# Kernel optimization log

Hardware: AMD Instinct MI355X
Metric: run time of the kernel (lower is better)

## Reference

```python
import jax, jax.numpy as jnp
import numpy as np

V, H, B = 64, 128, 16384  # num_visible, num_hidden = alpha*V, batch of spin configs
ISCALE = 0.001


def setup_inputs() -> dict:
    key = jax.random.key(0)
    k1, k2, k3, k4 = jax.random.split(key, 4)
    x = jax.random.normal(k1, (B, V), dtype=jnp.float32)
    weight_1 = jax.random.normal(k2, (V, H), dtype=jnp.float32) * ISCALE
    weight_2 = jax.random.normal(k3, (H, V, V), dtype=jnp.float32) * (ISCALE / 10.0)
    hidden_bias = jax.random.normal(k4, (H,), dtype=jnp.float32) * ISCALE
    return {"x": x, "weight_1": weight_1, "weight_2": weight_2, "hidden_bias": hidden_bias}


def reference(x, weight_1, weight_2, hidden_bias):
    b, v = x.shape
    h = weight_2.shape[0]
    # order-1 term: (B,V) @ (V,H) -> (B,H)
    w1 = x @ weight_1
    # order-2 term: outer product of spins per sample, contracted with weight_2.
    # vis_ij: (B,V,V) flattened to (B,V*V); weight_2 flattened to (H,V*V) -> GEMM.
    vis_ij = jnp.einsum('mi,mj->mij', x, x).reshape(b, v * v)
    w2 = (vis_ij @ weight_2.reshape(h, v * v).T) * 0.5
    act = jnp.cos(hidden_bias + w1 + w2)  # (B,H)
    psi = jnp.prod(act, axis=-1)          # (B,)
    return psi
```

## Files before the change

### kernel.cpp

```cpp
#include <hip/hip_runtime.h>
#include <hip/hip_bf16.h>
#include <cstdint>

#define NV 64
#define NH 128
#define NB 16384
#define NCHUNK 37
#define FRAG_ELEMS (NCHUNK * 8192)

typedef __bf16 bf16x8_t __attribute__((ext_vector_type(8)));
typedef float f32x4_t __attribute__((ext_vector_type(4)));
typedef float f32x2_t __attribute__((ext_vector_type(2)));
typedef uint32_t u32x4_t __attribute__((ext_vector_type(4)));
typedef uint32_t u32x2_t __attribute__((ext_vector_type(2)));

__device__ __forceinline__ uint32_t bf16_rne(float f) {
  uint32_t u = __float_as_uint(f);
  return (u + 0x7fffu + ((u >> 16) & 1u)) >> 16;
}

__global__ void cvt_kernel(const float* __restrict__ w1f,
                           const float* __restrict__ w2f,
                           uint16_t* __restrict__ frag) {
  int tg = blockIdx.x * 256 + threadIdx.x;
  int l = tg & 63, fh = (tg >> 6) & 7, c2 = tg >> 9;
  int chunk = c2 >> 1, jh = c2 & 1;
  int h = fh * 16 + (l & 15);
  int kb = jh * 32 + (l >> 4) * 8;
  uint32_t o16[8];
#pragma unroll
  for (int t = 0; t < 8; ++t) {
    int slot = kb + t;
    float v;
    if (chunk < 8) {
      int i = chunk * 8 + (slot >> 3), j = chunk * 8 + (slot & 7);
      v = 0.5f * w2f[h * 4096 + i * 64 + j];
    } else if (chunk < 36) {
      int o = chunk - 8, I = 0;
      while (o >= 7 - I) { o -= 7 - I; ++I; }
      int J = I + 1 + o;
      int i = I * 8 + (slot >> 3), j = J * 8 + (slot & 7);
      v = 0.5f * (w2f[h * 4096 + i * 64 + j] + w2f[h * 4096 + j * 64 + i]);
    } else {
      v = w1f[slot * 128 + h];
    }
    o16[t] = bf16_rne(v);
  }
  uint4 o;
  o.x = (o16[1] << 16) | o16[0];
  o.y = (o16[3] << 16) | o16[2];
  o.z = (o16[5] << 16) | o16[4];
  o.w = (o16[7] << 16) | o16[6];
  *(uint4*)(frag + ((size_t)(c2 * 8 + fh) << 9) + l * 8) = o;
}

__launch_bounds__(512, 2)
__global__ void rbm_kernel(const float* __restrict__ xg,
                           const float* __restrict__ biasg,
                           const __hip_bfloat16* __restrict__ frag,
                           float* __restrict__ outg) {
  __shared__ __align__(16) float xtile[64 * 76];
  __shared__ float part[4][64];

  const int tid  = threadIdx.x;
  const int wv   = tid >> 6;
  const int wm   = wv & 1;
  const int hq   = wv >> 1;
  const int lane = tid & 63;
  const int c15  = lane & 15;
  const int q    = lane >> 4;
  const int mblk = blockIdx.x * 64;

  constexpr int CI[36] = {0,1,2,3,4,5,6,7, 0,0,0,0,0,0,0, 1,1,1,1,1,1,
                          2,2,2,2,2, 3,3,3,3, 4,4,4, 5,5, 6};
  constexpr int CJ[36] = {0,1,2,3,4,5,6,7, 1,2,3,4,5,6,7, 2,3,4,5,6,7,
                          3,4,5,6,7, 4,5,6,7, 5,6,7, 6,7, 7};

  {
    int row = tid >> 3, grp = tid & 7;
    const float* p = xg + (size_t)(mblk + row) * NV + grp * 8;
    float4 a = *(const float4*)(p);
    float4 b = *(const float4*)(p + 4);
    *(float4*)(&xtile[row * 76 + grp * 8]) = a;
    *(float4*)(&xtile[row * 76 + grp * 8 + 4]) = b;
    xtile[row * 76 + 64 + grp] = 1.0f;
  }
  __syncthreads();

  const float* sx[2];
  f32x2_t xb[2][32];
#pragma unroll
  for (int im = 0; im < 2; ++im) {
    sx[im] = &xtile[(wm * 32 + im * 16 + c15) * 76];
#pragma unroll
    for (int g = 0; g < 8; ++g) {
      float4 a = *(const float4*)(sx[im] + g * 8);
      float4 b = *(const float4*)(sx[im] + g * 8 + 4);
      xb[im][g * 4 + 0] = f32x2_t{a.x, a.y};
      xb[im][g * 4 + 1] = f32x2_t{a.z, a.w};
      xb[im][g * 4 + 2] = f32x2_t{b.x, b.y};
      xb[im][g * 4 + 3] = f32x2_t{b.z, b.w};
    }
  }

  const __hip_bfloat16* pw = frag + (size_t)hq * 1024 + lane * 8;

  f32x4_t acc[2][2];
#pragma unroll
  for (int im = 0; im < 2; ++im)
#pragma unroll
    for (int ih = 0; ih < 2; ++ih)
      acc[im][ih] = (f32x4_t)0.0f;

  bf16x8_t bn[2][2];
#pragma unroll
  for (int jh = 0; jh < 2; ++jh)
#pragma unroll
    for (int ih = 0; ih < 2; ++ih)
      bn[jh][ih] = *(const bf16x8_t*)(pw + jh * 4096 + ih * 512);

#pragma unroll
  for (int c = 0; c < 36; ++c) {
    bf16x8_t bc[2][2];
#pragma unroll
    for (int jh = 0; jh < 2; ++jh)
#pragma unroll
      for (int ih = 0; ih < 2; ++ih)
        bc[jh][ih] = bn[jh][ih];
    {
      const __hip_bfloat16* pn = pw + (size_t)(c + 1) * 8192;
#pragma unroll
      for (int jh = 0; jh < 2; ++jh)
#pragma unroll
        for (int ih = 0; ih < 2; ++ih)
          bn[jh][ih] = *(const bf16x8_t*)(pn + jh * 4096 + ih * 512);
    }
    const int I = CI[c], J = CJ[c];
#pragma unroll
    for (int jh = 0; jh < 2; ++jh) {
      bf16x8_t afrag[2];
#pragma unroll
      for (int im = 0; im < 2; ++im) {
        float s = sx[im][I * 8 + jh * 4 + q];
        const f32x2_t s2 = f32x2_t{s, s};
        u32x4_t adv;
#pragma unroll
        for (int tt = 0; tt < 4; ++tt) {
          f32x2_t pr = s2 * xb[im][J * 4 + tt];
          u32x2_t u = __builtin_bit_cast(u32x2_t, pr);
          adv[tt] = __builtin_amdgcn_perm(u[1], u[0], 0x07060302);
        }
        afrag[im] = __builtin_bit_cast(bf16x8_t, adv);
      }
#pragma unroll
      for (int ih = 0; ih < 2; ++ih)
#pragma unroll
        for (int im = 0; im < 2; ++im)
          acc[im][ih] = __builtin_amdgcn_mfma_f32_16x16x32_bf16(
              afrag[im], bc[jh][ih], acc[im][ih], 0, 0, 0);
    }
  }

#pragma unroll
  for (int jh = 0; jh < 2; ++jh) {
    bf16x8_t afrag[2];
#pragma unroll
    for (int im = 0; im < 2; ++im) {
      float4 a = *(const float4*)(sx[im] + jh * 32 + q * 8);
      float4 b = *(const float4*)(sx[im] + jh * 32 + q * 8 + 4);
      const float pr[4][2] = {{a.x, a.y}, {a.z, a.w}, {b.x, b.y}, {b.z, b.w}};
      u32x4_t adv;
#pragma unroll
      for (int tt = 0; tt < 4; ++tt)
        adv[tt] = __builtin_amdgcn_perm(__float_as_uint(pr[tt][1]),
                                        __float_as_uint(pr[tt][0]), 0x07060302);
      afrag[im] = __builtin_bit_cast(bf16x8_t, adv);
    }
#pragma unroll
    for (int ih = 0; ih < 2; ++ih)
#pragma unroll
      for (int im = 0; im < 2; ++im)
        acc[im][ih] = __builtin_amdgcn_mfma_f32_16x16x32_bf16(
            afrag[im], bn[jh][ih], acc[im][ih], 0, 0, 0);
  }

  float bs[2];
#pragma unroll
  for (int ih = 0; ih < 2; ++ih)
    bs[ih] = biasg[hq * 32 + ih * 16 + c15];

  const float INV2PI = 0.15915494309189535f;
  float prod[2][4];
#pragma unroll
  for (int im = 0; im < 2; ++im)
#pragma unroll
    for (int r = 0; r < 4; ++r) {
      float c0 = __builtin_amdgcn_cosf((acc[im][0][r] + bs[0]) * INV2PI);
      float c1 = __builtin_amdgcn_cosf((acc[im][1][r] + bs[1]) * INV2PI);
      prod[im][r] = c0 * c1;
    }

#pragma unroll
  for (int ofs = 1; ofs < 16; ofs <<= 1)
#pragma unroll
    for (int im = 0; im < 2; ++im)
#pragma unroll
      for (int r = 0; r < 4; ++r)
        prod[im][r] *= __shfl_xor(prod[im][r], ofs, 16);

  if (c15 == 0) {
#pragma unroll
    for (int im = 0; im < 2; ++im)
#pragma unroll
      for (int r = 0; r < 4; ++r)
        part[hq][wm * 32 + im * 16 + q * 4 + r] = prod[im][r];
  }
  __syncthreads();
  if (tid < 64) {
    float f = part[0][tid] * part[1][tid] * part[2][tid] * part[3][tid];
    outg[mblk + tid] = f;
  }
}

extern "C" void kernel_launch(void* const* d_in, const int* in_sizes, int n_in,
                              void* d_out, int out_size, void* d_ws, size_t ws_size,
                              hipStream_t stream) {
  const float* x   = (const float*)d_in[0];
  const float* w1f = (const float*)d_in[1];
  const float* w2f = (const float*)d_in[2];
  const float* hb  = (const float*)d_in[3];
  float* out = (float*)d_out;
  uint16_t* frag = (uint16_t*)d_ws;
  (void)in_sizes; (void)n_in; (void)out_size; (void)ws_size;

  cvt_kernel<<<148, 256, 0, stream>>>(w1f, w2f, frag);
  rbm_kernel<<<NB / 64, 512, 0, stream>>>(
      x, hb, (const __hip_bfloat16*)frag, out);
}
```

Baseline: 85.98 us.

## Split-K across two blocks with 32x32 MFMA and separate cos-product reduction

The main kernel now splits the 37-chunk K dimension across two blocks per M tile using blockIdx.y. Each block uses 32x32x16 MFMA with a single accumulator, and partial sums go to a workspace buffer P. A third kernel adds the two partials and bias, applies cos, and does the row product with wave shuffles. The weight-conversion kernel stages each hidden unit's W2 slice in shared memory and writes a new fragment layout. This doubles grid parallelism and raises occupancy, at the cost of about 16 MB of extra partial-sum traffic and an extra kernel launch.

```diff
diff --git a/kernel.cpp b/kernel.cpp
--- a/kernel.cpp
+++ b/kernel.cpp
@@ -6,10 +6,9 @@
 #define NH 128
 #define NB 16384
 #define NCHUNK 37
-#define FRAG_ELEMS (NCHUNK * 8192)
 
 typedef __bf16 bf16x8_t __attribute__((ext_vector_type(8)));
-typedef float f32x4_t __attribute__((ext_vector_type(4)));
+typedef float f32x16_t __attribute__((ext_vector_type(16)));
 typedef float f32x2_t __attribute__((ext_vector_type(2)));
 typedef uint32_t u32x4_t __attribute__((ext_vector_type(4)));
 typedef uint32_t u32x2_t __attribute__((ext_vector_type(2)));
@@ -21,204 +20,173 @@
 
 __global__ void cvt_kernel(const float* __restrict__ w1f,
                            const float* __restrict__ w2f,
-                           uint16_t* __restrict__ frag) {
-  int tg = blockIdx.x * 256 + threadIdx.x;
-  int l = tg & 63, fh = (tg >> 6) & 7, c2 = tg >> 9;
-  int chunk = c2 >> 1, jh = c2 & 1;
-  int h = fh * 16 + (l & 15);
-  int kb = jh * 32 + (l >> 4) * 8;
-  uint32_t o16[8];
-#pragma unroll
-  for (int t = 0; t < 8; ++t) {
-    int slot = kb + t;
-    float v;
-    if (chunk < 8) {
-      int i = chunk * 8 + (slot >> 3), j = chunk * 8 + (slot & 7);
-      v = 0.5f * w2f[h * 4096 + i * 64 + j];
-    } else if (chunk < 36) {
-      int o = chunk - 8, I = 0;
+                           uint8_t* __restrict__ frag) {
+  __shared__ float W[4096];
+  __shared__ float w1c[64];
+  const int tid = threadIdx.x;
+  const int h = blockIdx.x;
+  {
+    const float* src = w2f + (size_t)h * 4096;
+#pragma unroll
+    for (int u = 0; u < 4; ++u)
+      *(float4*)(&W[u * 1024 + tid * 4]) =
+          *(const float4*)(src + u * 1024 + tid * 4);
+  }
+  if (tid < 64) w1c[tid] = w1f[tid * 128 + h];
+  __syncthreads();
+  const int fh2 = h >> 5, hl = h & 31;
+  for (int idx = tid; idx < 296; idx += 256) {
+    int c = idx >> 3, kk = (idx >> 1) & 3, lh = idx & 1;
+    int a = kk * 2 + lh;
+    float v[8];
+    if (c < 8) {
+      int ib = (c * 8 + a) * 64 + c * 8;
+#pragma unroll
+      for (int t = 0; t < 8; ++t) v[t] = 0.5f * W[ib + t];
+    } else if (c < 36) {
+      int o = c - 8, I = 0;
       while (o >= 7 - I) { o -= 7 - I; ++I; }
       int J = I + 1 + o;
-      int i = I * 8 + (slot >> 3), j = J * 8 + (slot & 7);
-      v = 0.5f * (w2f[h * 4096 + i * 64 + j] + w2f[h * 4096 + j * 64 + i]);
+      int i = I * 8 + a;
+#pragma unroll
+      for (int t = 0; t < 8; ++t) {
+        int j = J * 8 + t;
+        v[t] = 0.5f * (W[i * 64 + j] + W[j * 64 + i]);
+      }
     } else {
-      v = w1f[slot * 128 + h];
-    }
-    o16[t] = bf16_rne(v);
-  }
-  uint4 o;
-  o.x = (o16[1] << 16) | o16[0];
-  o.y = (o16[3] << 16) | o16[2];
-  o.z = (o16[5] << 16) | o16[4];
-  o.w = (o16[7] << 16) | o16[6];
-  *(uint4*)(frag + ((size_t)(c2 * 8 + fh) << 9) + l * 8) = o;
-}
-
-__launch_bounds__(512, 2)
-__global__ void rbm_kernel(const float* __restrict__ xg,
-                           const float* __restrict__ biasg,
-                           const __hip_bfloat16* __restrict__ frag,
-                           float* __restrict__ outg) {
-  __shared__ __align__(16) float xtile[64 * 76];
-  __shared__ float part[4][64];
-
-  const int tid  = threadIdx.x;
-  const int wv   = tid >> 6;
-  const int wm   = wv & 1;
-  const int hq   = wv >> 1;
-  const int lane = tid & 63;
-  const int c15  = lane & 15;
-  const int q    = lane >> 4;
-  const int mblk = blockIdx.x * 64;
-
+      int sb = kk * 16 + lh * 8;
+#pragma unroll
+      for (int t = 0; t < 8; ++t) v[t] = w1c[sb + t];
+    }
+    uint4 o4;
+    o4.x = (bf16_rne(v[1]) << 16) | bf16_rne(v[0]);
+    o4.y = (bf16_rne(v[3]) << 16) | bf16_rne(v[2]);
+    o4.z = (bf16_rne(v[5]) << 16) | bf16_rne(v[4]);
+    o4.w = (bf16_rne(v[7]) << 16) | bf16_rne(v[6]);
+    *(uint4*)(frag + ((size_t)((c * 4 + kk) * 4 + fh2) << 10) +
+              ((lh * 32 + hl) << 4)) = o4;
+  }
+}
+
+__device__ __forceinline__ uint32_t pack2(f32x2_t pr) {
+  u32x2_t u = __builtin_bit_cast(u32x2_t, pr);
+  return __builtin_amdgcn_perm(u[1], u[0], 0x07060302);
+}
+
+template <int C0, int C1>
+__device__ __forceinline__ void kloop(const uint8_t* pw, const f32x2_t* xb,
+                                      int lh, f32x16_t& acc, bf16x8_t* bn) {
   constexpr int CI[36] = {0,1,2,3,4,5,6,7, 0,0,0,0,0,0,0, 1,1,1,1,1,1,
                           2,2,2,2,2, 3,3,3,3, 4,4,4, 5,5, 6};
   constexpr int CJ[36] = {0,1,2,3,4,5,6,7, 1,2,3,4,5,6,7, 2,3,4,5,6,7,
                           3,4,5,6,7, 4,5,6,7, 5,6,7, 6,7, 7};
-
+#pragma unroll
+  for (int c = C0; c < C1; ++c) {
+    bf16x8_t bc[4];
+#pragma unroll
+    for (int kk = 0; kk < 4; ++kk) bc[kk] = bn[kk];
+    const uint8_t* pn = pw + (size_t)(c + 1) * 16384;
+#pragma unroll
+    for (int kk = 0; kk < 4; ++kk)
+      bn[kk] = *(const bf16x8_t*)(pn + kk * 4096);
+    const int I = CI[c], J = CJ[c];
+#pragma unroll
+    for (int kk = 0; kk < 4; ++kk) {
+      f32x2_t sp = xb[I * 4 + kk];
+      float s = lh ? sp.y : sp.x;
+      f32x2_t s2 = {s, s};
+      u32x4_t adv;
+#pragma unroll
+      for (int tt = 0; tt < 4; ++tt)
+        adv[tt] = pack2(s2 * xb[J * 4 + tt]);
+      acc = __builtin_amdgcn_mfma_f32_32x32x16_bf16(
+          __builtin_bit_cast(bf16x8_t, adv), bc[kk], acc, 0, 0, 0);
+    }
+  }
+}
+
+__launch_bounds__(512, 4)
+__global__ void rbm_main(const float* __restrict__ xg,
+                         const uint8_t* __restrict__ frag,
+                         float* __restrict__ P) {
+  const int tid = threadIdx.x;
+  const int wv = tid >> 6;
+  const int wm = wv & 1;
+  const int hq = wv >> 1;
+  const int lane = tid & 63;
+  const int l31 = lane & 31;
+  const int lh = lane >> 5;
+  const int mblk = blockIdx.x * 64;
+  const int ks = blockIdx.y;
+
+  f32x2_t xb[32];
   {
-    int row = tid >> 3, grp = tid & 7;
-    const float* p = xg + (size_t)(mblk + row) * NV + grp * 8;
-    float4 a = *(const float4*)(p);
-    float4 b = *(const float4*)(p + 4);
-    *(float4*)(&xtile[row * 76 + grp * 8]) = a;
-    *(float4*)(&xtile[row * 76 + grp * 8 + 4]) = b;
-    xtile[row * 76 + 64 + grp] = 1.0f;
-  }
-  __syncthreads();
-
-  const float* sx[2];
-  f32x2_t xb[2][32];
-#pragma unroll
-  for (int im = 0; im < 2; ++im) {
-    sx[im] = &xtile[(wm * 32 + im * 16 + c15) * 76];
-#pragma unroll
-    for (int g = 0; g < 8; ++g) {
-      float4 a = *(const float4*)(sx[im] + g * 8);
-      float4 b = *(const float4*)(sx[im] + g * 8 + 4);
-      xb[im][g * 4 + 0] = f32x2_t{a.x, a.y};
-      xb[im][g * 4 + 1] = f32x2_t{a.z, a.w};
-      xb[im][g * 4 + 2] = f32x2_t{b.x, b.y};
-      xb[im][g * 4 + 3] = f32x2_t{b.z, b.w};
-    }
-  }
-
-  const __hip_bfloat16* pw = frag + (size_t)hq * 1024 + lane * 8;
-
-  f32x4_t acc[2][2];
-#pragma unroll
-  for (int im = 0; im < 2; ++im)
-#pragma unroll
-    for (int ih = 0; ih < 2; ++ih)
-      acc[im][ih] = (f32x4_t)0.0f;
-
-  bf16x8_t bn[2][2];
-#pragma unroll
-  for (int jh = 0; jh < 2; ++jh)
-#pragma unroll
-    for (int ih = 0; ih < 2; ++ih)
-      bn[jh][ih] = *(const bf16x8_t*)(pw + jh * 4096 + ih * 512);
-
-#pragma unroll
-  for (int c = 0; c < 36; ++c) {
-    bf16x8_t bc[2][2];
-#pragma unroll
-    for (int jh = 0; jh < 2; ++jh)
-#pragma unroll
-      for (int ih = 0; ih < 2; ++ih)
-        bc[jh][ih] = bn[jh][ih];
-    {
-      const __hip_bfloat16* pn = pw + (size_t)(c + 1) * 8192;
-#pragma unroll
-      for (int jh = 0; jh < 2; ++jh)
-#pragma unroll
-        for (int ih = 0; ih < 2; ++ih)
-          bn[jh][ih] = *(const bf16x8_t*)(pn + jh * 4096 + ih * 512);
-    }
-    const int I = CI[c], J = CJ[c];
-#pragma unroll
-    for (int jh = 0; jh < 2; ++jh) {
-      bf16x8_t afrag[2];
-#pragma unroll
-      for (int im = 0; im < 2; ++im) {
-        float s = sx[im][I * 8 + jh * 4 + q];
-        const f32x2_t s2 = f32x2_t{s, s};
-        u32x4_t adv;
-#pragma unroll
-        for (int tt = 0; tt < 4; ++tt) {
-          f32x2_t pr = s2 * xb[im][J * 4 + tt];
-          u32x2_t u = __builtin_bit_cast(u32x2_t, pr);
-          adv[tt] = __builtin_amdgcn_perm(u[1], u[0], 0x07060302);
-        }
-        afrag[im] = __builtin_bit_cast(bf16x8_t, adv);
+    const float* p = xg + (size_t)(mblk + wm * 32 + l31) * NV;
+#pragma unroll
+    for (int g = 0; g < 16; ++g) {
+      float4 v = *(const float4*)(p + g * 4);
+      xb[g * 2] = f32x2_t{v.x, v.y};
+      xb[g * 2 + 1] = f32x2_t{v.z, v.w};
+    }
+  }
+
+  const uint8_t* pw = frag + hq * 1024 + (size_t)lane * 16;
+  f32x16_t acc = (f32x16_t)0.0f;
+  bf16x8_t bn[4];
+  {
+    const uint8_t* p0 = pw + (size_t)(ks ? 18 : 0) * 16384;
+#pragma unroll
+    for (int kk = 0; kk < 4; ++kk)
+      bn[kk] = *(const bf16x8_t*)(p0 + kk * 4096);
+  }
+
+  if (ks == 0) {
+    kloop<0, 18>(pw, xb, lh, acc, bn);
+  } else {
+    kloop<18, 36>(pw, xb, lh, acc, bn);
+#pragma unroll
+    for (int kk = 0; kk < 4; ++kk) {
+      u32x4_t adv;
+#pragma unroll
+      for (int tt = 0; tt < 4; ++tt) {
+        f32x2_t v = lh ? xb[kk * 8 + 4 + tt] : xb[kk * 8 + tt];
+        adv[tt] = pack2(v);
       }
-#pragma unroll
-      for (int ih = 0; ih < 2; ++ih)
-#pragma unroll
-        for (int im = 0; im < 2; ++im)
-          acc[im][ih] = __builtin_amdgcn_mfma_f32_16x16x32_bf16(
-              afrag[im], bc[jh][ih], acc[im][ih], 0, 0, 0);
-    }
-  }
-
-#pragma unroll
-  for (int jh = 0; jh < 2; ++jh) {
-    bf16x8_t afrag[2];
-#pragma unroll
-    for (int im = 0; im < 2; ++im) {
-      float4 a = *(const float4*)(sx[im] + jh * 32 + q * 8);
-      float4 b = *(const float4*)(sx[im] + jh * 32 + q * 8 + 4);
-      const float pr[4][2] = {{a.x, a.y}, {a.z, a.w}, {b.x, b.y}, {b.z, b.w}};
-      u32x4_t adv;
-#pragma unroll
-      for (int tt = 0; tt < 4; ++tt)
-        adv[tt] = __builtin_amdgcn_perm(__float_as_uint(pr[tt][1]),
-                                        __float_as_uint(pr[tt][0]), 0x07060302);
-      afrag[im] = __builtin_bit_cast(bf16x8_t, adv);
-    }
-#pragma unroll
-    for (int ih = 0; ih < 2; ++ih)
-#pragma unroll
-      for (int im = 0; im < 2; ++im)
-        acc[im][ih] = __builtin_amdgcn_mfma_f32_16x16x32_bf16(
-            afrag[im], bn[jh][ih], acc[im][ih], 0, 0, 0);
-  }
-
-  float bs[2];
-#pragma unroll
-  for (int ih = 0; ih < 2; ++ih)
-    bs[ih] = biasg[hq * 32 + ih * 16 + c15];
-
+      acc = __builtin_amdgcn_mfma_f32_32x32x16_bf16(
+          __builtin_bit_cast(bf16x8_t, adv), bn[kk], acc, 0, 0, 0);
+    }
+  }
+
+  float* pp = P + ((size_t)(ks * NB + mblk + wm * 32)) * NH + hq * 32 + l31;
+#pragma unroll
+  for (int r = 0; r < 16; ++r) {
+    int mloc = (r & 3) + 8 * (r >> 2) + 4 * lh;
+    pp[(size_t)mloc * NH] = acc[r];
+  }
+}
+
+__global__ void reduce_kernel(const float* __restrict__ P,
+                              const float* __restrict__ biasg,
+                              float* __restrict__ outg) {
+  const int tid = threadIdx.x;
+  const int wv = tid >> 6;
+  const int lane = tid & 63;
+  const int m0 = blockIdx.x * 16 + wv * 4;
+  const float b0 = biasg[lane], b1 = biasg[64 + lane];
   const float INV2PI = 0.15915494309189535f;
-  float prod[2][4];
-#pragma unroll
-  for (int im = 0; im < 2; ++im)
-#pragma unroll
-    for (int r = 0; r < 4; ++r) {
-      float c0 = __builtin_amdgcn_cosf((acc[im][0][r] + bs[0]) * INV2PI);
-      float c1 = __builtin_amdgcn_cosf((acc[im][1][r] + bs[1]) * INV2PI);
-      prod[im][r] = c0 * c1;
-    }
-
-#pragma unroll
-  for (int ofs = 1; ofs < 16; ofs <<= 1)
-#pragma unroll
-    for (int im = 0; im < 2; ++im)
-#pragma unroll
-      for (int r = 0; r < 4; ++r)
-        prod[im][r] *= __shfl_xor(prod[im][r], ofs, 16);
-
-  if (c15 == 0) {
-#pragma unroll
-    for (int im = 0; im < 2; ++im)
-#pragma unroll
-      for (int r = 0; r < 4; ++r)
-        part[hq][wm * 32 + im * 16 + q * 4 + r] = prod[im][r];
-  }
-  __syncthreads();
-  if (tid < 64) {
-    float f = part[0][tid] * part[1][tid] * part[2][tid] * part[3][tid];
-    outg[mblk + tid] = f;
+#pragma unroll
+  for (int u = 0; u < 4; ++u) {
+    const int m = m0 + u;
+    const float* p0 = P + (size_t)m * NH;
+    const float* p1 = P + (size_t)(NB + m) * NH;
+    float a0 = p0[lane] + p1[lane] + b0;
+    float a1 = p0[64 + lane] + p1[64 + lane] + b1;
+    float pr = __builtin_amdgcn_cosf(a0 * INV2PI) *
+               __builtin_amdgcn_cosf(a1 * INV2PI);
+#pragma unroll
+    for (int ofs = 1; ofs < 64; ofs <<= 1)
+      pr *= __shfl_xor(pr, ofs, 64);
+    if (lane == 0) outg[m] = pr;
   }
 }
 
@@ -230,10 +198,11 @@
   const float* w2f = (const float*)d_in[2];
   const float* hb  = (const float*)d_in[3];
   float* out = (float*)d_out;
-  uint16_t* frag = (uint16_t*)d_ws;
+  uint8_t* frag = (uint8_t*)d_ws;
+  float* P = (float*)((uint8_t*)d_ws + (1 << 20));
   (void)in_sizes; (void)n_in; (void)out_size; (void)ws_size;
 
-  cvt_kernel<<<148, 256, 0, stream>>>(w1f, w2f, frag);
-  rbm_kernel<<<NB / 64, 512, 0, stream>>>(
-      x, hb, (const __hip_bfloat16*)frag, out);
-}
+  cvt_kernel<<<128, 256, 0, stream>>>(w1f, w2f, frag);
+  rbm_main<<<dim3(NB / 64, 2), 512, 0, stream>>>(x, frag, P);
+  reduce_kernel<<<NB / 16, 256, 0, stream>>>(P, hb, out);
+}
```

Result: slower. 96.20 us (+11.9%).
